# Optimization experiments

Hardware: AMD Instinct MI355X
Metric: run time of the kernel (lower is better)

## Reference

```python
import jax, jax.numpy as jnp
import numpy as np

N_NODES = 100_000
N_EDGES = 3_200_000
F_IN, F_HID, F_OUT = 128, 128, 128
MLP_HID, MLP_OUT = 256, 64


def setup_inputs() -> dict:
    key = jax.random.key(0)
    ks = jax.random.split(key, 11)
    def w(k, shape):
        fan_in = shape[0]
        return jax.random.normal(k, shape, jnp.float32) / jnp.sqrt(jnp.float32(fan_in))
    return {
        'x':   jax.random.normal(ks[0], (N_NODES, F_IN), jnp.float32),
        'src': jax.random.randint(ks[1], (N_EDGES,), 0, N_NODES, jnp.int32),
        'dst': jax.random.randint(ks[2], (N_EDGES,), 0, N_NODES, jnp.int32),
        'w1':  w(ks[3], (F_IN, F_HID)),  'b1': jnp.zeros((F_HID,), jnp.float32),
        'w2':  w(ks[4], (F_HID, F_OUT)), 'b2': jnp.zeros((F_OUT,), jnp.float32),
        'wm1': w(ks[5], (F_OUT, MLP_HID)), 'bm1': jnp.zeros((MLP_HID,), jnp.float32),
        'wm2': w(ks[6], (MLP_HID, MLP_OUT)), 'bm2': jnp.zeros((MLP_OUT,), jnp.float32),
    }


def reference(x, src, dst, w1, b1, w2, b2, wm1, bm1, wm2, bm2):
    n = x.shape[0]
    ones = jnp.ones(src.shape[0], x.dtype)
    # DGL GraphConv norm='both': clamp degrees to >=1, symmetric D^-1/2 A D^-1/2
    out_norm = jnp.clip(jax.ops.segment_sum(ones, src, num_segments=n), 1.0) ** -0.5
    in_norm = jnp.clip(jax.ops.segment_sum(ones, dst, num_segments=n), 1.0) ** -0.5

    def gconv(h, w, b):
        msg = (h * out_norm[:, None])[src]                       # [E, F] gather
        agg = jax.ops.segment_sum(msg, dst, num_segments=n)      # [N, F] scatter-add
        return (agg * in_norm[:, None]) @ w + b

    h = jax.nn.relu(gconv(x, w1, b1))   # conv1 + relu (dropout is identity in eval)
    h = jax.nn.relu(gconv(h, w2, b2))   # conv2 + relu
    h = jax.nn.relu(h @ wm1 + bm1)      # MLP hidden layer
    return h @ wm2 + bm2                # MLP output (no final activation)
```

## Files before the change

### kernel.cpp

```cpp
#include <hip/hip_runtime.h>
#include <hip/hip_bf16.h>
#include <cstdint>

__device__ __forceinline__ unsigned short f2b(float f) {
    union { float f; unsigned int i; } v; v.f = f;
    unsigned int i = v.i;
    unsigned int r = (i + 0x7FFFu + ((i >> 16) & 1u)) >> 16;
    return (unsigned short)r;
}
__device__ __forceinline__ float b2f_lo(unsigned int p) {
    union { unsigned int i; float f; } v; v.i = p << 16; return v.f;
}
__device__ __forceinline__ float b2f_hi(unsigned int p) {
    union { unsigned int i; float f; } v; v.i = p & 0xFFFF0000u; return v.f;
}
__device__ __forceinline__ unsigned int pack2(float a, float b) {
    return (unsigned int)f2b(a) | ((unsigned int)f2b(b) << 16);
}

typedef __attribute__((__ext_vector_type__(8))) __bf16 bf16x8;
typedef __attribute__((__ext_vector_type__(4))) float  f32x4;

#define N_NODES 100000
#define N_EDGES 3200000
#define NBUCK   200
#define BSZ     500

__global__ void k_hist2(const int* __restrict__ src, const int* __restrict__ dst,
                        int* __restrict__ gcntA, int* __restrict__ gcntB, int E) {
    __shared__ int hA[NBUCK], hB[NBUCK];
    int t = threadIdx.x;
    if (t < NBUCK) { hA[t] = 0; hB[t] = 0; }
    __syncthreads();
    for (int i = blockIdx.x * blockDim.x + t; i < E; i += gridDim.x * blockDim.x) {
        atomicAdd(&hA[dst[i] / BSZ], 1);
        atomicAdd(&hB[src[i] / BSZ], 1);
    }
    __syncthreads();
    if (t < NBUCK) {
        if (hA[t]) atomicAdd(&gcntA[t], hA[t]);
        if (hB[t]) atomicAdd(&gcntB[t], hB[t]);
    }
}

__global__ void k_scan_coarse(const int* __restrict__ gcntA, const int* __restrict__ gcntB,
                              int* __restrict__ gbaseA, int* __restrict__ gbaseB,
                              int* __restrict__ gcurA, int* __restrict__ gcurB,
                              int* __restrict__ offsets) {
    __shared__ int pA[256], pB[256];
    int t = threadIdx.x;
    int vA = (t < NBUCK) ? gcntA[t] : 0;
    int vB = (t < NBUCK) ? gcntB[t] : 0;
    pA[t] = vA; pB[t] = vB;
    __syncthreads();
    for (int d = 1; d < 256; d <<= 1) {
        int a = (t >= d) ? pA[t - d] : 0;
        int b = (t >= d) ? pB[t - d] : 0;
        __syncthreads();
        pA[t] += a; pB[t] += b;
        __syncthreads();
    }
    if (t < NBUCK) {
        gbaseA[t] = pA[t] - vA; gcurA[t] = pA[t] - vA;
        gbaseB[t] = pB[t] - vB; gcurB[t] = pB[t] - vB;
    }
    if (t == 255) {
        gbaseA[NBUCK] = pA[255];
        gbaseB[NBUCK] = pB[255];
        offsets[N_NODES] = pA[255];
    }
}

__global__ void k_scatter(const int* __restrict__ src, const int* __restrict__ dst,
                          int* __restrict__ gcurA, int* __restrict__ gcurB,
                          uint2* __restrict__ pairs, int* __restrict__ keysB, int E) {
    __shared__ int hA[NBUCK], hB[NBUCK], baA[NBUCK], baB[NBUCK], lcA[NBUCK], lcB[NBUCK];
    int t = threadIdx.x;
    const int CHUNK = 12500;
    int lo = blockIdx.x * CHUNK, hi = min(lo + CHUNK, E);
    if (t < NBUCK) { hA[t] = 0; hB[t] = 0; }
    __syncthreads();
    for (int i = lo + t; i < hi; i += 256) {
        atomicAdd(&hA[dst[i] / BSZ], 1);
        atomicAdd(&hB[src[i] / BSZ], 1);
    }
    __syncthreads();
    if (t < NBUCK) {
        baA[t] = hA[t] ? atomicAdd(&gcurA[t], hA[t]) : 0;
        lcA[t] = 0;
        baB[t] = hB[t] ? atomicAdd(&gcurB[t], hB[t]) : 0;
        lcB[t] = 0;
    }
    __syncthreads();
    for (int i = lo + t; i < hi; i += 256) {
        int s = src[i], d = dst[i];
        int bA = d / BSZ;
        int l  = atomicAdd(&lcA[bA], 1);
        pairs[baA[bA] + l] = make_uint2((unsigned)s, (unsigned)d);
        int bB = s / BSZ;
        int l2 = atomicAdd(&lcB[bB], 1);
        keysB[baB[bB] + l2] = s;
    }
}

__global__ void k_csr_bucket(const uint2* __restrict__ pairs, const int* __restrict__ gbaseA,
                             int* __restrict__ offsets, float* __restrict__ in_norm,
                             int* __restrict__ esrc) {
    __shared__ int hist[512], scan[512], curs[512];
    int b = blockIdx.x, t = threadIdx.x;
    int node0 = b * BSZ;
    int bstart = gbaseA[b], bend = gbaseA[b + 1];
    if (t < 512) hist[t] = 0;
    __syncthreads();
    for (int i = bstart + t; i < bend; i += 1024)
        atomicAdd(&hist[(int)pairs[i].y - node0], 1);
    __syncthreads();
    if (t < 512) scan[t] = hist[t];
    __syncthreads();
    for (int d = 1; d < 512; d <<= 1) {
        int v = (t < 512 && t >= d) ? scan[t - d] : 0;
        __syncthreads();
        if (t < 512) scan[t] += v;
        __syncthreads();
    }
    if (t < BSZ) {
        int excl = scan[t] - hist[t];
        offsets[node0 + t] = bstart + excl;
        in_norm[node0 + t] = rsqrtf((float)max(hist[t], 1));
        curs[t] = excl;
    }
    __syncthreads();
    for (int i = bstart + t; i < bend; i += 1024) {
        uint2 p = pairs[i];
        int d = (int)p.y - node0;
        int l = atomicAdd(&curs[d], 1);
        esrc[bstart + l] = (int)p.x;
    }
}

__global__ void k_sortwave(const int* __restrict__ offsets, int* __restrict__ esrc, int N) {
    int node = blockIdx.x * 4 + (threadIdx.x >> 6);
    if (node >= N) return;
    int lane = threadIdx.x & 63;
    int lo = offsets[node], hi = offsets[node + 1];
    int len = hi - lo;
    if (len <= 1) return;
    const int INF = 0x7FFFFFFF;
    int v0 = (lane < len) ? esrc[lo + lane] : INF;
    int v1 = (64 + lane < len) ? esrc[lo + 64 + lane] : INF;
#pragma unroll
    for (int k = 2; k <= 128; k <<= 1) {
#pragma unroll
        for (int d = 64; d > 0; d >>= 1) {
            if (d >= k) continue;
            if (d == 64) {
                int a = min(v0, v1), b = max(v0, v1);
                v0 = a; v1 = b;
            } else {
                int w0 = __shfl_xor(v0, d, 64);
                int w1 = __shfl_xor(v1, d, 64);
                bool up0 = ((lane & k) == 0);
                bool up1 = (((64 + lane) & k) == 0);
                bool lower = ((lane & d) == 0);
                v0 = (lower == up0) ? min(v0, w0) : max(v0, w0);
                v1 = (lower == up1) ? min(v1, w1) : max(v1, w1);
            }
        }
    }
    if (lane < len) esrc[lo + lane] = v0;
    if (64 + lane < len) esrc[lo + 64 + lane] = v1;
}

__global__ void k_count_bucket(const int* __restrict__ keys, const int* __restrict__ gbaseB,
                               float* __restrict__ out_norm) {
    __shared__ int hist[512];
    int b = blockIdx.x, t = threadIdx.x;
    int node0 = b * BSZ;
    int bstart = gbaseB[b], bend = gbaseB[b + 1];
    if (t < 512) hist[t] = 0;
    __syncthreads();
    for (int i = bstart + t; i < bend; i += 1024)
        atomicAdd(&hist[keys[i] - node0], 1);
    __syncthreads();
    if (t < BSZ) out_norm[node0 + t] = rsqrtf((float)max(hist[t], 1));
}

__global__ void k_scale(const float4* __restrict__ x4, const float* __restrict__ out_norm,
                        uint2* __restrict__ xs, int total4) {
    int i = blockIdx.x * blockDim.x + threadIdx.x;
    if (i < total4) {
        int node = i >> 5;
        float on = out_norm[node];
        float4 v = x4[i];
        uint2 o;
        o.x = pack2(v.x * on, v.y * on);
        o.y = pack2(v.z * on, v.w * on);
        xs[i] = o;
    }
}

__global__ void k_transpose4(const float* __restrict__ w1, const float* __restrict__ w2,
                             const float* __restrict__ wm1, const float* __restrict__ wm2,
                             unsigned short* __restrict__ t1, unsigned short* __restrict__ t2,
                             unsigned short* __restrict__ tm1, unsigned short* __restrict__ tm2) {
    int i = blockIdx.x * blockDim.x + threadIdx.x;
    const float* w; unsigned short* t; int N, idx;
    if (i < 16384)       { w = w1;  t = t1;  N = 128; idx = i; }
    else if (i < 32768)  { w = w2;  t = t2;  N = 128; idx = i - 16384; }
    else if (i < 65536)  { w = wm1; t = tm1; N = 256; idx = i - 32768; }
    else if (i < 81920)  { w = wm2; t = tm2; N = 64;  idx = i - 65536; }
    else return;
    int K = (i < 65536) ? 128 : 256;
    int k = idx / N, n = idx - k * N;
    t[(size_t)n * K + k] = f2b(w[idx]);
}

#define AGG_NODE_BODY(node)                                                     \
    int lo = offsets[node], hi = offsets[node + 1];                             \
    float a0 = 0.f, a1 = 0.f, a2 = 0.f, a3 = 0.f,                               \
          a4 = 0.f, a5 = 0.f, a6 = 0.f, a7 = 0.f;                               \
    int k = lo + g;                                                             \
    for (; k + 12 < hi; k += 16) {                                              \
        int s0 = esrc[k];                                                       \
        int s1 = esrc[k + 4];                                                   \
        int s2 = esrc[k + 8];                                                   \
        int s3 = esrc[k + 12];                                                  \
        uint4 p0 = feat[(size_t)s0 * 16 + c];                                   \
        uint4 p1 = feat[(size_t)s1 * 16 + c];                                   \
        uint4 p2 = feat[(size_t)s2 * 16 + c];                                   \
        uint4 p3 = feat[(size_t)s3 * 16 + c];                                   \
        a0 += b2f_lo(p0.x); a1 += b2f_hi(p0.x);                                 \
        a2 += b2f_lo(p0.y); a3 += b2f_hi(p0.y);                                 \
        a4 += b2f_lo(p0.z); a5 += b2f_hi(p0.z);                                 \
        a6 += b2f_lo(p0.w); a7 += b2f_hi(p0.w);                                 \
        a0 += b2f_lo(p1.x); a1 += b2f_hi(p1.x);                                 \
        a2 += b2f_lo(p1.y); a3 += b2f_hi(p1.y);                                 \
        a4 += b2f_lo(p1.z); a5 += b2f_hi(p1.z);                                 \
        a6 += b2f_lo(p1.w); a7 += b2f_hi(p1.w);                                 \
        a0 += b2f_lo(p2.x); a1 += b2f_hi(p2.x);                                 \
        a2 += b2f_lo(p2.y); a3 += b2f_hi(p2.y);                                 \
        a4 += b2f_lo(p2.z); a5 += b2f_hi(p2.z);                                 \
        a6 += b2f_lo(p2.w); a7 += b2f_hi(p2.w);                                 \
        a0 += b2f_lo(p3.x); a1 += b2f_hi(p3.x);                                 \
        a2 += b2f_lo(p3.y); a3 += b2f_hi(p3.y);                                 \
        a4 += b2f_lo(p3.z); a5 += b2f_hi(p3.z);                                 \
        a6 += b2f_lo(p3.w); a7 += b2f_hi(p3.w);                                 \
    }                                                                           \
    for (; k < hi; k += 4) {                                                    \
        int s = esrc[k];                                                        \
        uint4 p = feat[(size_t)s * 16 + c];                                     \
        a0 += b2f_lo(p.x); a1 += b2f_hi(p.x);                                   \
        a2 += b2f_lo(p.y); a3 += b2f_hi(p.y);                                   \
        a4 += b2f_lo(p.z); a5 += b2f_hi(p.z);                                   \
        a6 += b2f_lo(p.w); a7 += b2f_hi(p.w);                                   \
    }                                                                           \
    a0 += __shfl_xor(a0, 16, 64); a0 += __shfl_xor(a0, 32, 64);                 \
    a1 += __shfl_xor(a1, 16, 64); a1 += __shfl_xor(a1, 32, 64);                 \
    a2 += __shfl_xor(a2, 16, 64); a2 += __shfl_xor(a2, 32, 64);                 \
    a3 += __shfl_xor(a3, 16, 64); a3 += __shfl_xor(a3, 32, 64);                 \
    a4 += __shfl_xor(a4, 16, 64); a4 += __shfl_xor(a4, 32, 64);                 \
    a5 += __shfl_xor(a5, 16, 64); a5 += __shfl_xor(a5, 32, 64);                 \
    a6 += __shfl_xor(a6, 16, 64); a6 += __shfl_xor(a6, 32, 64);                 \
    a7 += __shfl_xor(a7, 16, 64); a7 += __shfl_xor(a7, 32, 64);

__global__ void k_conv(const int* __restrict__ offsets, const int* __restrict__ esrc,
                       const uint4* __restrict__ feat, const float* __restrict__ in_norm,
                       const unsigned short* __restrict__ WT, const float* __restrict__ bias,
                       const float* __restrict__ row_scale, unsigned short* __restrict__ C,
                       int N) {
    __shared__ unsigned short A[32][136];
    int wv = threadIdx.x >> 6, lane = threadIdx.x & 63;
    int row0 = blockIdx.x * 32;
    int g = lane >> 4, c = lane & 15;

    for (int i = 0; i < 8; ++i) {
        int nl = wv * 8 + i;
        int node = row0 + nl;
        AGG_NODE_BODY(node)
        if (g == 0) {
            float inn = in_norm[node];
            uint4 o;
            o.x = pack2(a0 * inn, a1 * inn);
            o.y = pack2(a2 * inn, a3 * inn);
            o.z = pack2(a4 * inn, a5 * inn);
            o.w = pack2(a6 * inn, a7 * inn);
            *(uint4*)&A[nl][c * 8] = o;
        }
    }
    __syncthreads();

    int m = lane & 15, q = lane >> 4;
    const unsigned short* b0 = WT + (size_t)(wv * 32 + m) * 128 + q * 8;
    const unsigned short* b1 = b0 + (size_t)16 * 128;
    f32x4 acc00 = {0.f, 0.f, 0.f, 0.f}, acc10 = {0.f, 0.f, 0.f, 0.f};
    f32x4 acc01 = {0.f, 0.f, 0.f, 0.f}, acc11 = {0.f, 0.f, 0.f, 0.f};
#pragma unroll
    for (int k = 0; k < 128; k += 32) {
        bf16x8 bf0 = *(const bf16x8*)(b0 + k);
        bf16x8 bf1 = *(const bf16x8*)(b1 + k);
        bf16x8 af0 = *(const bf16x8*)&A[m][q * 8 + k];
        bf16x8 af1 = *(const bf16x8*)&A[16 + m][q * 8 + k];
        acc00 = __builtin_amdgcn_mfma_f32_16x16x32_bf16(af0, bf0, acc00, 0, 0, 0);
        acc10 = __builtin_amdgcn_mfma_f32_16x16x32_bf16(af1, bf0, acc10, 0, 0, 0);
        acc01 = __builtin_amdgcn_mfma_f32_16x16x32_bf16(af0, bf1, acc01, 0, 0, 0);
        acc11 = __builtin_amdgcn_mfma_f32_16x16x32_bf16(af1, bf1, acc11, 0, 0, 0);
    }
    int col0 = wv * 32 + m;
    int col1 = col0 + 16;
    float bc0 = bias[col0], bc1 = bias[col1];
#pragma unroll
    for (int r = 0; r < 4; r++) {
        int rr = row0 + q * 4 + r;
        int rr1 = rr + 16;
        float v00 = fmaxf(acc00[r] + bc0, 0.f);
        float v10 = fmaxf(acc10[r] + bc0, 0.f);
        float v01 = fmaxf(acc01[r] + bc1, 0.f);
        float v11 = fmaxf(acc11[r] + bc1, 0.f);
        if (row_scale) {
            float s0 = row_scale[rr], s1 = row_scale[rr1];
            v00 *= s0; v01 *= s0; v10 *= s1; v11 *= s1;
        }
        C[(size_t)rr * 128 + col0]  = f2b(v00);
        C[(size_t)rr * 128 + col1]  = f2b(v01);
        C[(size_t)rr1 * 128 + col0] = f2b(v10);
        C[(size_t)rr1 * 128 + col1] = f2b(v11);
    }
}

__global__ void k_conv2_mlp(const int* __restrict__ offsets, const int* __restrict__ esrc,
                            const uint4* __restrict__ feat, const float* __restrict__ in_norm,
                            const unsigned short* __restrict__ WT2, const float* __restrict__ b2,
                            const unsigned short* __restrict__ WTM1, const float* __restrict__ bm1,
                            const unsigned short* __restrict__ WTM2, const float* __restrict__ bm2,
                            float* __restrict__ out, int N) {
    __shared__ unsigned short smem[12800];
    unsigned short (*H1)[136] = (unsigned short(*)[136])(smem);
    unsigned short (*A)[136]  = (unsigned short(*)[136])(smem + 4352);
    unsigned short (*H2)[264] = (unsigned short(*)[264])(smem + 4352);

    int wv = threadIdx.x >> 6, lane = threadIdx.x & 63;
    int row0 = blockIdx.x * 32;
    int g = lane >> 4, c = lane & 15;

    for (int i = 0; i < 8; ++i) {
        int nl = wv * 8 + i;
        int node = row0 + nl;
        AGG_NODE_BODY(node)
        if (g == 0) {
            float inn = in_norm[node];
            uint4 o;
            o.x = pack2(a0 * inn, a1 * inn);
            o.y = pack2(a2 * inn, a3 * inn);
            o.z = pack2(a4 * inn, a5 * inn);
            o.w = pack2(a6 * inn, a7 * inn);
            *(uint4*)&A[nl][c * 8] = o;
        }
    }
    __syncthreads();

    int m = lane & 15, q = lane >> 4;

    {
        const unsigned short* b0 = WT2 + (size_t)(wv * 32 + m) * 128 + q * 8;
        const unsigned short* b1 = b0 + (size_t)16 * 128;
        f32x4 acc00 = {0.f, 0.f, 0.f, 0.f}, acc10 = {0.f, 0.f, 0.f, 0.f};
        f32x4 acc01 = {0.f, 0.f, 0.f, 0.f}, acc11 = {0.f, 0.f, 0.f, 0.f};
#pragma unroll
        for (int k = 0; k < 128; k += 32) {
            bf16x8 bf0 = *(const bf16x8*)(b0 + k);
            bf16x8 bf1 = *(const bf16x8*)(b1 + k);
            bf16x8 af0 = *(const bf16x8*)&A[m][q * 8 + k];
            bf16x8 af1 = *(const bf16x8*)&A[16 + m][q * 8 + k];
            acc00 = __builtin_amdgcn_mfma_f32_16x16x32_bf16(af0, bf0, acc00, 0, 0, 0);
            acc10 = __builtin_amdgcn_mfma_f32_16x16x32_bf16(af1, bf0, acc10, 0, 0, 0);
            acc01 = __builtin_amdgcn_mfma_f32_16x16x32_bf16(af0, bf1, acc01, 0, 0, 0);
            acc11 = __builtin_amdgcn_mfma_f32_16x16x32_bf16(af1, bf1, acc11, 0, 0, 0);
        }
        __syncthreads();
        int col0 = wv * 32 + m;
        int col1 = col0 + 16;
        float bc0 = b2[col0], bc1 = b2[col1];
#pragma unroll
        for (int r = 0; r < 4; r++) {
            int rl = q * 4 + r;
            H1[rl][col0]      = f2b(fmaxf(acc00[r] + bc0, 0.f));
            H1[rl][col1]      = f2b(fmaxf(acc01[r] + bc1, 0.f));
            H1[rl + 16][col0] = f2b(fmaxf(acc10[r] + bc0, 0.f));
            H1[rl + 16][col1] = f2b(fmaxf(acc11[r] + bc1, 0.f));
        }
    }
    __syncthreads();

#pragma unroll
    for (int cb = 0; cb < 4; cb++) {
        int colh = wv * 64 + cb * 16 + m;
        const unsigned short* bp = WTM1 + (size_t)colh * 128 + q * 8;
        f32x4 acc0 = {0.f, 0.f, 0.f, 0.f};
        f32x4 acc1 = {0.f, 0.f, 0.f, 0.f};
#pragma unroll
        for (int s = 0; s < 4; s++) {
            bf16x8 bfr = *(const bf16x8*)(bp + s * 32);
            bf16x8 ha0 = *(const bf16x8*)&H1[m][s * 32 + q * 8];
            bf16x8 ha1 = *(const bf16x8*)&H1[m + 16][s * 32 + q * 8];
            acc0 = __builtin_amdgcn_mfma_f32_16x16x32_bf16(ha0, bfr, acc0, 0, 0, 0);
            acc1 = __builtin_amdgcn_mfma_f32_16x16x32_bf16(ha1, bfr, acc1, 0, 0, 0);
        }
        float bc = bm1[colh];
#pragma unroll
        for (int r = 0; r < 4; r++) {
            H2[q * 4 + r][colh]      = f2b(fmaxf(acc0[r] + bc, 0.f));
            H2[q * 4 + r + 16][colh] = f2b(fmaxf(acc1[r] + bc, 0.f));
        }
    }
    __syncthreads();

    {
        int colo = wv * 16 + m;
        const unsigned short* bp2 = WTM2 + (size_t)colo * 256 + q * 8;
        f32x4 acc0 = {0.f, 0.f, 0.f, 0.f};
        f32x4 acc1 = {0.f, 0.f, 0.f, 0.f};
#pragma unroll
        for (int s = 0; s < 8; s++) {
            bf16x8 bfr = *(const bf16x8*)(bp2 + s * 32);
            bf16x8 ha0 = *(const bf16x8*)&H2[m][s * 32 + q * 8];
            bf16x8 ha1 = *(const bf16x8*)&H2[m + 16][s * 32 + q * 8];
            acc0 = __builtin_amdgcn_mfma_f32_16x16x32_bf16(ha0, bfr, acc0, 0, 0, 0);
            acc1 = __builtin_amdgcn_mfma_f32_16x16x32_bf16(ha1, bfr, acc1, 0, 0, 0);
        }
        float bc = bm2[colo];
#pragma unroll
        for (int r = 0; r < 4; r++) {
            out[(size_t)(row0 + q * 4 + r) * 64 + colo]      = acc0[r] + bc;
            out[(size_t)(row0 + q * 4 + r + 16) * 64 + colo] = acc1[r] + bc;
        }
    }
}

extern "C" void kernel_launch(void* const* d_in, const int* in_sizes, int n_in,
                              void* d_out, int out_size, void* d_ws, size_t ws_size,
                              hipStream_t stream) {
    const float* x    = (const float*)d_in[0];
    const int*   src  = (const int*)d_in[1];
    const int*   dst  = (const int*)d_in[2];
    const float* w1   = (const float*)d_in[3];
    const float* b1   = (const float*)d_in[4];
    const float* w2   = (const float*)d_in[5];
    const float* b2   = (const float*)d_in[6];
    const float* wm1  = (const float*)d_in[7];
    const float* bm1  = (const float*)d_in[8];
    const float* wm2  = (const float*)d_in[9];
    const float* bm2  = (const float*)d_in[10];

    const int N = N_NODES;
    const int E = N_EDGES;

    char* p = (char*)d_ws;
    auto alloc = [&](size_t bytes) -> void* {
        void* r = (void*)p;
        p += (bytes + 255) & ~(size_t)255;
        return r;
    };
    int*   gcntA   = (int*)alloc(256 * 4);
    int*   gcntB   = (int*)alloc(256 * 4);
    int*   gbaseA  = (int*)alloc(256 * 4);
    int*   gbaseB  = (int*)alloc(256 * 4);
    int*   gcurA   = (int*)alloc(256 * 4);
    int*   gcurB   = (int*)alloc(256 * 4);
    int*   offsets = (int*)alloc((size_t)(N + 1) * 4);
    float* out_norm = (float*)alloc((size_t)N * 4);
    float* in_norm  = (float*)alloc((size_t)N * 4);
    int*   esrc     = (int*)alloc((size_t)E * 4);
    unsigned int* bufA = (unsigned int*)alloc((size_t)N * 128 * 2);
    unsigned int* bufB = (unsigned int*)alloc((size_t)N * 128 * 2);
    unsigned int* bufC = (unsigned int*)alloc((size_t)N * 128 * 2);
    unsigned short* wt1  = (unsigned short*)alloc(128 * 128 * 2);
    unsigned short* wt2  = (unsigned short*)alloc(128 * 128 * 2);
    unsigned short* wtm1 = (unsigned short*)alloc(256 * 128 * 2);
    unsigned short* wtm2 = (unsigned short*)alloc(64 * 256 * 2);
    (void)ws_size; (void)n_in; (void)in_sizes; (void)out_size;

    uint2* pairs = (uint2*)bufB;
    int*   keysB = (int*)bufC;

    hipMemsetAsync(gcntA, 0, 256 * 4, stream);
    hipMemsetAsync(gcntB, 0, 256 * 4, stream);

    const int TB = 256;
    k_hist2<<<dim3(256), dim3(TB), 0, stream>>>(src, dst, gcntA, gcntB, E);
    k_scan_coarse<<<dim3(1), dim3(TB), 0, stream>>>(gcntA, gcntB, gbaseA, gbaseB,
                                                    gcurA, gcurB, offsets);
    k_scatter<<<dim3(256), dim3(TB), 0, stream>>>(src, dst, gcurA, gcurB, pairs, keysB, E);
    k_csr_bucket<<<dim3(NBUCK), dim3(1024), 0, stream>>>(pairs, gbaseA, offsets, in_norm, esrc);
    k_sortwave<<<dim3(N / 4), dim3(TB), 0, stream>>>(offsets, esrc, N);
    k_count_bucket<<<dim3(NBUCK), dim3(1024), 0, stream>>>(keysB, gbaseB, out_norm);

    k_scale<<<dim3((N * 32 + TB - 1) / TB), dim3(TB), 0, stream>>>(
        (const float4*)x, out_norm, (uint2*)bufA, N * 32);
    k_transpose4<<<dim3(320), dim3(TB), 0, stream>>>(w1, w2, wm1, wm2, wt1, wt2, wtm1, wtm2);

    k_conv<<<dim3(N / 32), dim3(TB), 0, stream>>>(
        offsets, esrc, (const uint4*)bufA, in_norm, wt1, b1, out_norm,
        (unsigned short*)bufC, N);

    k_conv2_mlp<<<dim3(N / 32), dim3(TB), 0, stream>>>(
        offsets, esrc, (const uint4*)bufC, in_norm, wt2, b2, wtm1, bm1, wtm2, bm2,
        (float*)d_out, N);
}
```

Measured before the change: 599.9 us.

## Compute out-degree with global atomics, pack edge pairs, shrink MLP shared memory

Replaces the src-bucket scatter and count pass with direct global atomic increments into a per-node degree array. The out-norm is now computed inside the scale kernel, which drops the keysB writes and the k_count_bucket launch. Edge pairs are packed into one 32-bit word (local dst offset and src), halving the scatter and bucket traffic. The conv2+MLP kernel splits the 256-wide hidden layer into two halves to shrink shared memory from 25.6KB to 17.4KB, and both conv kernels get launch_bounds(256,8) for higher occupancy; this adds global atomic contention on deg and extra barriers.

Result: slower. 645.2 us (+7.5%).

```diff
diff --git a/kernel.cpp b/kernel.cpp
--- a/kernel.cpp
+++ b/kernel.cpp
@@ -27,83 +27,65 @@
 #define BSZ     500
 
 __global__ void k_hist2(const int* __restrict__ src, const int* __restrict__ dst,
-                        int* __restrict__ gcntA, int* __restrict__ gcntB, int E) {
-    __shared__ int hA[NBUCK], hB[NBUCK];
+                        int* __restrict__ gcntA, int* __restrict__ deg, int E) {
+    __shared__ int hA[NBUCK];
     int t = threadIdx.x;
-    if (t < NBUCK) { hA[t] = 0; hB[t] = 0; }
+    if (t < NBUCK) hA[t] = 0;
     __syncthreads();
     for (int i = blockIdx.x * blockDim.x + t; i < E; i += gridDim.x * blockDim.x) {
         atomicAdd(&hA[dst[i] / BSZ], 1);
-        atomicAdd(&hB[src[i] / BSZ], 1);
-    }
-    __syncthreads();
-    if (t < NBUCK) {
-        if (hA[t]) atomicAdd(&gcntA[t], hA[t]);
-        if (hB[t]) atomicAdd(&gcntB[t], hB[t]);
-    }
-}
-
-__global__ void k_scan_coarse(const int* __restrict__ gcntA, const int* __restrict__ gcntB,
-                              int* __restrict__ gbaseA, int* __restrict__ gbaseB,
-                              int* __restrict__ gcurA, int* __restrict__ gcurB,
+        atomicAdd(&deg[src[i]], 1);
+    }
+    __syncthreads();
+    if (t < NBUCK && hA[t]) atomicAdd(&gcntA[t], hA[t]);
+}
+
+__global__ void k_scan_coarse(const int* __restrict__ gcntA,
+                              int* __restrict__ gbaseA, int* __restrict__ gcurA,
                               int* __restrict__ offsets) {
-    __shared__ int pA[256], pB[256];
+    __shared__ int pA[256];
     int t = threadIdx.x;
     int vA = (t < NBUCK) ? gcntA[t] : 0;
-    int vB = (t < NBUCK) ? gcntB[t] : 0;
-    pA[t] = vA; pB[t] = vB;
+    pA[t] = vA;
     __syncthreads();
     for (int d = 1; d < 256; d <<= 1) {
         int a = (t >= d) ? pA[t - d] : 0;
-        int b = (t >= d) ? pB[t - d] : 0;
-        __syncthreads();
-        pA[t] += a; pB[t] += b;
-        __syncthreads();
-    }
-    if (t < NBUCK) {
-        gbaseA[t] = pA[t] - vA; gcurA[t] = pA[t] - vA;
-        gbaseB[t] = pB[t] - vB; gcurB[t] = pB[t] - vB;
-    }
+        __syncthreads();
+        pA[t] += a;
+        __syncthreads();
+    }
+    if (t < NBUCK) { gbaseA[t] = pA[t] - vA; gcurA[t] = pA[t] - vA; }
     if (t == 255) {
         gbaseA[NBUCK] = pA[255];
-        gbaseB[NBUCK] = pB[255];
         offsets[N_NODES] = pA[255];
     }
 }
 
 __global__ void k_scatter(const int* __restrict__ src, const int* __restrict__ dst,
-                          int* __restrict__ gcurA, int* __restrict__ gcurB,
-                          uint2* __restrict__ pairs, int* __restrict__ keysB, int E) {
-    __shared__ int hA[NBUCK], hB[NBUCK], baA[NBUCK], baB[NBUCK], lcA[NBUCK], lcB[NBUCK];
+                          int* __restrict__ gcurA, unsigned* __restrict__ pairs, int E) {
+    __shared__ int hA[NBUCK], baA[NBUCK], lcA[NBUCK];
     int t = threadIdx.x;
     const int CHUNK = 12500;
     int lo = blockIdx.x * CHUNK, hi = min(lo + CHUNK, E);
-    if (t < NBUCK) { hA[t] = 0; hB[t] = 0; }
-    __syncthreads();
-    for (int i = lo + t; i < hi; i += 256) {
+    if (t < NBUCK) hA[t] = 0;
+    __syncthreads();
+    for (int i = lo + t; i < hi; i += 256)
         atomicAdd(&hA[dst[i] / BSZ], 1);
-        atomicAdd(&hB[src[i] / BSZ], 1);
-    }
     __syncthreads();
     if (t < NBUCK) {
         baA[t] = hA[t] ? atomicAdd(&gcurA[t], hA[t]) : 0;
         lcA[t] = 0;
-        baB[t] = hB[t] ? atomicAdd(&gcurB[t], hB[t]) : 0;
-        lcB[t] = 0;
     }
     __syncthreads();
     for (int i = lo + t; i < hi; i += 256) {
         int s = src[i], d = dst[i];
         int bA = d / BSZ;
         int l  = atomicAdd(&lcA[bA], 1);
-        pairs[baA[bA] + l] = make_uint2((unsigned)s, (unsigned)d);
-        int bB = s / BSZ;
-        int l2 = atomicAdd(&lcB[bB], 1);
-        keysB[baB[bB] + l2] = s;
-    }
-}
-
-__global__ void k_csr_bucket(const uint2* __restrict__ pairs, const int* __restrict__ gbaseA,
+        pairs[baA[bA] + l] = ((unsigned)(d - bA * BSZ) << 17) | (unsigned)s;
+    }
+}
+
+__global__ void k_csr_bucket(const unsigned* __restrict__ pairs, const int* __restrict__ gbaseA,
                              int* __restrict__ offsets, float* __restrict__ in_norm,
                              int* __restrict__ esrc) {
     __shared__ int hist[512], scan[512], curs[512];
@@ -113,7 +95,7 @@
     if (t < 512) hist[t] = 0;
     __syncthreads();
     for (int i = bstart + t; i < bend; i += 1024)
-        atomicAdd(&hist[(int)pairs[i].y - node0], 1);
+        atomicAdd(&hist[pairs[i] >> 17], 1);
     __syncthreads();
     if (t < 512) scan[t] = hist[t];
     __syncthreads();
@@ -131,10 +113,10 @@
     }
     __syncthreads();
     for (int i = bstart + t; i < bend; i += 1024) {
-        uint2 p = pairs[i];
-        int d = (int)p.y - node0;
+        unsigned p = pairs[i];
+        int d = (int)(p >> 17);
         int l = atomicAdd(&curs[d], 1);
-        esrc[bstart + l] = (int)p.x;
+        esrc[bstart + l] = (int)(p & 0x1FFFFu);
     }
 }
 
@@ -171,31 +153,18 @@
     if (64 + lane < len) esrc[lo + 64 + lane] = v1;
 }
 
-__global__ void k_count_bucket(const int* __restrict__ keys, const int* __restrict__ gbaseB,
-                               float* __restrict__ out_norm) {
-    __shared__ int hist[512];
-    int b = blockIdx.x, t = threadIdx.x;
-    int node0 = b * BSZ;
-    int bstart = gbaseB[b], bend = gbaseB[b + 1];
-    if (t < 512) hist[t] = 0;
-    __syncthreads();
-    for (int i = bstart + t; i < bend; i += 1024)
-        atomicAdd(&hist[keys[i] - node0], 1);
-    __syncthreads();
-    if (t < BSZ) out_norm[node0 + t] = rsqrtf((float)max(hist[t], 1));
-}
-
-__global__ void k_scale(const float4* __restrict__ x4, const float* __restrict__ out_norm,
-                        uint2* __restrict__ xs, int total4) {
+__global__ void k_scale(const float4* __restrict__ x4, const int* __restrict__ deg,
+                        float* __restrict__ out_norm, uint2* __restrict__ xs, int total4) {
     int i = blockIdx.x * blockDim.x + threadIdx.x;
     if (i < total4) {
         int node = i >> 5;
-        float on = out_norm[node];
+        float on = rsqrtf((float)max(deg[node], 1));
         float4 v = x4[i];
         uint2 o;
         o.x = pack2(v.x * on, v.y * on);
         o.y = pack2(v.z * on, v.w * on);
         xs[i] = o;
+        if ((i & 31) == 0) out_norm[node] = on;
     }
 }
 
@@ -263,11 +232,12 @@
     a6 += __shfl_xor(a6, 16, 64); a6 += __shfl_xor(a6, 32, 64);                 \
     a7 += __shfl_xor(a7, 16, 64); a7 += __shfl_xor(a7, 32, 64);
 
-__global__ void k_conv(const int* __restrict__ offsets, const int* __restrict__ esrc,
-                       const uint4* __restrict__ feat, const float* __restrict__ in_norm,
-                       const unsigned short* __restrict__ WT, const float* __restrict__ bias,
-                       const float* __restrict__ row_scale, unsigned short* __restrict__ C,
-                       int N) {
+__global__ __launch_bounds__(256, 8)
+void k_conv(const int* __restrict__ offsets, const int* __restrict__ esrc,
+            const uint4* __restrict__ feat, const float* __restrict__ in_norm,
+            const unsigned short* __restrict__ WT, const float* __restrict__ bias,
+            const float* __restrict__ row_scale, unsigned short* __restrict__ C,
+            int N) {
     __shared__ unsigned short A[32][136];
     int wv = threadIdx.x >> 6, lane = threadIdx.x & 63;
     int row0 = blockIdx.x * 32;
@@ -316,10 +286,8 @@
         float v10 = fmaxf(acc10[r] + bc0, 0.f);
         float v01 = fmaxf(acc01[r] + bc1, 0.f);
         float v11 = fmaxf(acc11[r] + bc1, 0.f);
-        if (row_scale) {
-            float s0 = row_scale[rr], s1 = row_scale[rr1];
-            v00 *= s0; v01 *= s0; v10 *= s1; v11 *= s1;
-        }
+        float s0 = row_scale[rr], s1 = row_scale[rr1];
+        v00 *= s0; v01 *= s0; v10 *= s1; v11 *= s1;
         C[(size_t)rr * 128 + col0]  = f2b(v00);
         C[(size_t)rr * 128 + col1]  = f2b(v01);
         C[(size_t)rr1 * 128 + col0] = f2b(v10);
@@ -327,16 +295,17 @@
     }
 }
 
-__global__ void k_conv2_mlp(const int* __restrict__ offsets, const int* __restrict__ esrc,
-                            const uint4* __restrict__ feat, const float* __restrict__ in_norm,
-                            const unsigned short* __restrict__ WT2, const float* __restrict__ b2,
-                            const unsigned short* __restrict__ WTM1, const float* __restrict__ bm1,
-                            const unsigned short* __restrict__ WTM2, const float* __restrict__ bm2,
-                            float* __restrict__ out, int N) {
-    __shared__ unsigned short smem[12800];
+__global__ __launch_bounds__(256, 8)
+void k_conv2_mlp(const int* __restrict__ offsets, const int* __restrict__ esrc,
+                 const uint4* __restrict__ feat, const float* __restrict__ in_norm,
+                 const unsigned short* __restrict__ WT2, const float* __restrict__ b2,
+                 const unsigned short* __restrict__ WTM1, const float* __restrict__ bm1,
+                 const unsigned short* __restrict__ WTM2, const float* __restrict__ bm2,
+                 float* __restrict__ out, int N) {
+    __shared__ unsigned short smem[8704];
     unsigned short (*H1)[136] = (unsigned short(*)[136])(smem);
     unsigned short (*A)[136]  = (unsigned short(*)[136])(smem + 4352);
-    unsigned short (*H2)[264] = (unsigned short(*)[264])(smem + 4352);
+    unsigned short (*H2)[136] = (unsigned short(*)[136])(smem + 4352);
 
     int wv = threadIdx.x >> 6, lane = threadIdx.x & 63;
     int row0 = blockIdx.x * 32;
@@ -361,14 +330,14 @@
     int m = lane & 15, q = lane >> 4;
 
     {
-        const unsigned short* b0 = WT2 + (size_t)(wv * 32 + m) * 128 + q * 8;
-        const unsigned short* b1 = b0 + (size_t)16 * 128;
+        const unsigned short* bb0 = WT2 + (size_t)(wv * 32 + m) * 128 + q * 8;
+        const unsigned short* bb1 = bb0 + (size_t)16 * 128;
         f32x4 acc00 = {0.f, 0.f, 0.f, 0.f}, acc10 = {0.f, 0.f, 0.f, 0.f};
         f32x4 acc01 = {0.f, 0.f, 0.f, 0.f}, acc11 = {0.f, 0.f, 0.f, 0.f};
 #pragma unroll
         for (int k = 0; k < 128; k += 32) {
-            bf16x8 bf0 = *(const bf16x8*)(b0 + k);
-            bf16x8 bf1 = *(const bf16x8*)(b1 + k);
+            bf16x8 bf0 = *(const bf16x8*)(bb0 + k);
+            bf16x8 bf1 = *(const bf16x8*)(bb1 + k);
             bf16x8 af0 = *(const bf16x8*)&A[m][q * 8 + k];
             bf16x8 af1 = *(const bf16x8*)&A[16 + m][q * 8 + k];
             acc00 = __builtin_amdgcn_mfma_f32_16x16x32_bf16(af0, bf0, acc00, 0, 0, 0);
@@ -376,7 +345,6 @@
             acc01 = __builtin_amdgcn_mfma_f32_16x16x32_bf16(af0, bf1, acc01, 0, 0, 0);
             acc11 = __builtin_amdgcn_mfma_f32_16x16x32_bf16(af1, bf1, acc11, 0, 0, 0);
         }
-        __syncthreads();
         int col0 = wv * 32 + m;
         int col1 = col0 + 16;
         float bc0 = b2[col0], bc1 = b2[col1];
@@ -391,48 +359,50 @@
     }
     __syncthreads();
 
-#pragma unroll
-    for (int cb = 0; cb < 4; cb++) {
-        int colh = wv * 64 + cb * 16 + m;
-        const unsigned short* bp = WTM1 + (size_t)colh * 128 + q * 8;
-        f32x4 acc0 = {0.f, 0.f, 0.f, 0.f};
-        f32x4 acc1 = {0.f, 0.f, 0.f, 0.f};
+    f32x4 macc0 = {0.f, 0.f, 0.f, 0.f}, macc1 = {0.f, 0.f, 0.f, 0.f};
+    int colo = wv * 16 + m;
+    const unsigned short* bp2 = WTM2 + (size_t)colo * 256 + q * 8;
+#pragma unroll
+    for (int half = 0; half < 2; ++half) {
+#pragma unroll
+        for (int cb = 0; cb < 2; cb++) {
+            int colh = half * 128 + wv * 32 + cb * 16 + m;
+            const unsigned short* bp = WTM1 + (size_t)colh * 128 + q * 8;
+            f32x4 acc0 = {0.f, 0.f, 0.f, 0.f};
+            f32x4 acc1 = {0.f, 0.f, 0.f, 0.f};
+#pragma unroll
+            for (int s = 0; s < 4; s++) {
+                bf16x8 bfr = *(const bf16x8*)(bp + s * 32);
+                bf16x8 ha0 = *(const bf16x8*)&H1[m][s * 32 + q * 8];
+                bf16x8 ha1 = *(const bf16x8*)&H1[m + 16][s * 32 + q * 8];
+                acc0 = __builtin_amdgcn_mfma_f32_16x16x32_bf16(ha0, bfr, acc0, 0, 0, 0);
+                acc1 = __builtin_amdgcn_mfma_f32_16x16x32_bf16(ha1, bfr, acc1, 0, 0, 0);
+            }
+            float bc = bm1[colh];
+            int cl = colh & 127;
+#pragma unroll
+            for (int r = 0; r < 4; r++) {
+                H2[q * 4 + r][cl]      = f2b(fmaxf(acc0[r] + bc, 0.f));
+                H2[q * 4 + r + 16][cl] = f2b(fmaxf(acc1[r] + bc, 0.f));
+            }
+        }
+        __syncthreads();
 #pragma unroll
         for (int s = 0; s < 4; s++) {
-            bf16x8 bfr = *(const bf16x8*)(bp + s * 32);
-            bf16x8 ha0 = *(const bf16x8*)&H1[m][s * 32 + q * 8];
-            bf16x8 ha1 = *(const bf16x8*)&H1[m + 16][s * 32 + q * 8];
-            acc0 = __builtin_amdgcn_mfma_f32_16x16x32_bf16(ha0, bfr, acc0, 0, 0, 0);
-            acc1 = __builtin_amdgcn_mfma_f32_16x16x32_bf16(ha1, bfr, acc1, 0, 0, 0);
-        }
-        float bc = bm1[colh];
-#pragma unroll
-        for (int r = 0; r < 4; r++) {
-            H2[q * 4 + r][colh]      = f2b(fmaxf(acc0[r] + bc, 0.f));
-            H2[q * 4 + r + 16][colh] = f2b(fmaxf(acc1[r] + bc, 0.f));
-        }
-    }
-    __syncthreads();
-
-    {
-        int colo = wv * 16 + m;
-        const unsigned short* bp2 = WTM2 + (size_t)colo * 256 + q * 8;
-        f32x4 acc0 = {0.f, 0.f, 0.f, 0.f};
-        f32x4 acc1 = {0.f, 0.f, 0.f, 0.f};
-#pragma unroll
-        for (int s = 0; s < 8; s++) {
-            bf16x8 bfr = *(const bf16x8*)(bp2 + s * 32);
+            bf16x8 bfr = *(const bf16x8*)(bp2 + half * 128 + s * 32);
             bf16x8 ha0 = *(const bf16x8*)&H2[m][s * 32 + q * 8];
             bf16x8 ha1 = *(const bf16x8*)&H2[m + 16][s * 32 + q * 8];
-            acc0 = __builtin_amdgcn_mfma_f32_16x16x32_bf16(ha0, bfr, acc0, 0, 0, 0);
-            acc1 = __builtin_amdgcn_mfma_f32_16x16x32_bf16(ha1, bfr, acc1, 0, 0, 0);
-        }
-        float bc = bm2[colo];
-#pragma unroll
-        for (int r = 0; r < 4; r++) {
-            out[(size_t)(row0 + q * 4 + r) * 64 + colo]      = acc0[r] + bc;
-            out[(size_t)(row0 + q * 4 + r + 16) * 64 + colo] = acc1[r] + bc;
-        }
+            macc0 = __builtin_amdgcn_mfma_f32_16x16x32_bf16(ha0, bfr, macc0, 0, 0, 0);
+            macc1 = __builtin_amdgcn_mfma_f32_16x16x32_bf16(ha1, bfr, macc1, 0, 0, 0);
+        }
+        __syncthreads();
+    }
+
+    float bc = bm2[colo];
+#pragma unroll
+    for (int r = 0; r < 4; r++) {
+        out[(size_t)(row0 + q * 4 + r) * 64 + colo]      = macc0[r] + bc;
+        out[(size_t)(row0 + q * 4 + r + 16) * 64 + colo] = macc1[r] + bc;
     }
 }
 
@@ -461,11 +431,9 @@
         return r;
     };
     int*   gcntA   = (int*)alloc(256 * 4);
-    int*   gcntB   = (int*)alloc(256 * 4);
+    int*   deg     = (int*)alloc((size_t)N * 4);
     int*   gbaseA  = (int*)alloc(256 * 4);
-    int*   gbaseB  = (int*)alloc(256 * 4);
     int*   gcurA   = (int*)alloc(256 * 4);
-    int*   gcurB   = (int*)alloc(256 * 4);
     int*   offsets = (int*)alloc((size_t)(N + 1) * 4);
     float* out_norm = (float*)alloc((size_t)N * 4);
     float* in_norm  = (float*)alloc((size_t)N * 4);
@@ -479,23 +447,19 @@
     unsigned short* wtm2 = (unsigned short*)alloc(64 * 256 * 2);
     (void)ws_size; (void)n_in; (void)in_sizes; (void)out_size;
 
-    uint2* pairs = (uint2*)bufB;
-    int*   keysB = (int*)bufC;
-
-    hipMemsetAsync(gcntA, 0, 256 * 4, stream);
-    hipMemsetAsync(gcntB, 0, 256 * 4, stream);
+    unsigned* pairs = (unsigned*)bufB;
+
+    hipMemsetAsync(gcntA, 0, 256 * 4 + (size_t)N * 4, stream);
 
     const int TB = 256;
-    k_hist2<<<dim3(256), dim3(TB), 0, stream>>>(src, dst, gcntA, gcntB, E);
-    k_scan_coarse<<<dim3(1), dim3(TB), 0, stream>>>(gcntA, gcntB, gbaseA, gbaseB,
-                                                    gcurA, gcurB, offsets);
-    k_scatter<<<dim3(256), dim3(TB), 0, stream>>>(src, dst, gcurA, gcurB, pairs, keysB, E);
+    k_hist2<<<dim3(256), dim3(TB), 0, stream>>>(src, dst, gcntA, deg, E);
+    k_scan_coarse<<<dim3(1), dim3(TB), 0, stream>>>(gcntA, gbaseA, gcurA, offsets);
+    k_scatter<<<dim3(256), dim3(TB), 0, stream>>>(src, dst, gcurA, pairs, E);
     k_csr_bucket<<<dim3(NBUCK), dim3(1024), 0, stream>>>(pairs, gbaseA, offsets, in_norm, esrc);
     k_sortwave<<<dim3(N / 4), dim3(TB), 0, stream>>>(offsets, esrc, N);
-    k_count_bucket<<<dim3(NBUCK), dim3(1024), 0, stream>>>(keysB, gbaseB, out_norm);
 
     k_scale<<<dim3((N * 32 + TB - 1) / TB), dim3(TB), 0, stream>>>(
-        (const float4*)x, out_norm, (uint2*)bufA, N * 32);
+        (const float4*)x, deg, out_norm, (uint2*)bufA, N * 32);
     k_transpose4<<<dim3(320), dim3(TB), 0, stream>>>(w1, w2, wm1, wm2, wt1, wt2, wtm1, wtm2);
 
     k_conv<<<dim3(N / 32), dim3(TB), 0, stream>>>(
```
